# Performance work log

Measured on AMD Instinct MI355X. Metric: run time of the kernel, lower is better.

## Reference

```python
import jax, jax.numpy as jnp
import numpy as np

SIGMA_DATA = 16.0
ALPHA_BOND = 1.0


def safe_norm(x, axis=-1):
    # L2 norm with zero (sub)gradient at 0, matching torch.norm's behavior
    sq = jnp.sum(x * x, axis=axis)
    n = jnp.sqrt(jnp.where(sq > 0, sq, 1.0))
    return jnp.where(sq > 0, n, 0.0)


def weighted_rigid_align(x_l, xGT_l, w_l):
    # Aligns x_l onto xGT_l's frame (Kabsch with weights); output is detached.
    wm = w_l[..., None]                                   # [B,N,1]
    denom = jnp.sum(wm, axis=1, keepdims=True)
    mu = jnp.sum(wm * x_l, axis=1, keepdims=True) / denom
    muGT = jnp.sum(wm * xGT_l, axis=1, keepdims=True) / denom
    xc = x_l - mu
    xGTc = xGT_l - muGT
    # M = (w * xGT_c)^T @ x_c  -> [B,3,3]
    M = jnp.einsum('bni,bnj->bij', wm * xGTc, xc)
    U, S, Vh = jnp.linalg.svd(M)
    R = U @ Vh
    det = jnp.linalg.det(R)
    Fm = jnp.array([[1.0, 0.0, 0.0], [0.0, 1.0, 0.0], [0.0, 0.0, -1.0]], dtype=R.dtype)
    Rfix = jnp.einsum('bij,jk,bkl->bil', U, Fm, Vh)
    R = jnp.where(det[:, None, None] < 0, Rfix, R)
    xalign = xc @ jnp.swapaxes(R, -1, -2) + muGT
    return jax.lax.stop_gradient(xalign)


def diffusion_loss(xpred_l, xGT_l, ht, w_l):
    # Align ground truth onto prediction (note arg order in original forward)
    xGT_aligned = weighted_rigid_align(xGT_l, xpred_l, w_l)
    loss = jnp.sum(safe_norm(xpred_l - xGT_aligned) * w_l) / jnp.sum(w_l)
    if ALPHA_BOND > 0:
        w_pair = w_l[:, :, None] * w_l[:, None, :]                 # [B,N,N]
        d_pred = safe_norm(xpred_l[:, :, None] - xpred_l[:, None]) # [B,N,N]
        d_gt = safe_norm(xGT_l[:, :, None] - xGT_l[:, None])       # [B,N,N]
        L_bond = w_pair * (d_pred - d_gt) ** 2
        loss = loss + ALPHA_BOND * jnp.sum(L_bond) / jnp.sum(w_pair)
    return (ht ** 2 + SIGMA_DATA ** 2) / (ht + SIGMA_DATA) ** 2 * loss


def setup_inputs() -> dict:
    key = jax.random.key(0)
    k1, k2, k3, k4 = jax.random.split(key, 4)
    B, N = 4, 2048
    xpred_l = jax.random.normal(k1, (B, N, 3), dtype=jnp.float32) * 10.0
    xGT_l = jax.random.normal(k2, (B, N, 3), dtype=jnp.float32) * 10.0
    ht = jax.random.uniform(k3, (B,), dtype=jnp.float32, minval=0.1, maxval=4.0)
    w_l = jax.random.uniform(k4, (B, N), dtype=jnp.float32, minval=0.1, maxval=1.0)
    return {"xpred_l": xpred_l, "xGT_l": xGT_l, "ht": ht, "w_l": w_l}


def reference(xpred_l, xGT_l, ht, w_l):
    return diffusion_loss(xpred_l, xGT_l, ht, w_l)
```

## Files before the change

### kernel.cpp

```cpp
#include <hip/hip_runtime.h>
#include <math.h>


#define RT 256
#define CT 128
#define MAXB 8

__global__ __launch_bounds__(RT, 4)
void k_bond_stats(const float* __restrict__ pred, const float* __restrict__ gt,
                  const float* __restrict__ w, double* __restrict__ ws,
                  int N, int B, unsigned total) {
    const int b    = blockIdx.z;
    const int bx   = blockIdx.x;
    const int r0   = bx * RT;
    const int c0   = blockIdx.y * CT;
    const int tid  = threadIdx.x;
    const int lane = tid & 63, wave = tid >> 6;
    const int GX   = gridDim.x;
    const unsigned linear = (blockIdx.z * gridDim.y + blockIdx.y) * GX + blockIdx.x;

    double* statsSlot = ws;
    double* bondSlot  = ws + (size_t)B * GX * 16;

    if (blockIdx.x == 0 && blockIdx.y == 0 && blockIdx.z == 0 && tid == 0) {
        double* fin = bondSlot + total;
        fin[0] = 0.0; fin[1] = 0.0; fin[2] = 0.0;
    }

    const float* p  = pred + (size_t)b * N * 3;
    const float* g  = gt   + (size_t)b * N * 3;
    const float* wb = w    + (size_t)b * N;

    __shared__ float4 sp4[CT], sg4[CT];
    __shared__ double shred[4][16];

    const int  n      = r0 + tid;
    const bool row_ok = (n < N);
    float px=0.f,py=0.f,pz=0.f,gx=0.f,gy=0.f,gz=0.f,wn=0.f;
    if (row_ok) {
        px = p[3*n]; py = p[3*n+1]; pz = p[3*n+2];
        gx = g[3*n]; gy = g[3*n+1]; gz = g[3*n+2];
        wn = wb[n];
    }

    const bool bond_active = (c0 + CT > r0 + 1) && (c0 < N);
    float bond_f = 0.0f;
    if (bond_active) {
        for (int i = tid; i < CT; i += RT) {
            int m = c0 + i;
            float4 a = make_float4(0.f,0.f,0.f,0.f), c = a;
            if (m < N) {
                a = make_float4(p[3*m], p[3*m+1], p[3*m+2], wb[m]);
                c = make_float4(g[3*m], g[3*m+1], g[3*m+2], 0.f);
            }
            sp4[i] = a; sg4[i] = c;
        }
        __syncthreads();
        if (row_ok) {
            const int cc = min(CT, N - c0);
            if (c0 >= r0 + RT) {
                #pragma unroll 4
                for (int i = 0; i < cc; i++) {
                    float4 cp = sp4[i], cg = sg4[i];
                    float dxp=px-cp.x, dyp=py-cp.y, dzp=pz-cp.z;
                    float dxg=gx-cg.x, dyg=gy-cg.y, dzg=gz-cg.z;
                    float dp = sqrtf(dxp*dxp+dyp*dyp+dzp*dzp);
                    float dg = sqrtf(dxg*dxg+dyg*dyg+dzg*dzg);
                    float dd = dp - dg;
                    bond_f += (wn*cp.w)*(dd*dd);
                }
            } else if (n < c0 + cc - 1) {
                #pragma unroll 4
                for (int i = 0; i < cc; i++) {
                    float4 cp = sp4[i], cg = sg4[i];
                    float dxp=px-cp.x, dyp=py-cp.y, dzp=pz-cp.z;
                    float dxg=gx-cg.x, dyg=gy-cg.y, dzg=gz-cg.z;
                    float dp = sqrtf(dxp*dxp+dyp*dyp+dzp*dzp);
                    float dg = sqrtf(dxg*dxg+dyg*dyg+dzg*dzg);
                    float dd = dp - dg;
                    float t  = (wn*cp.w)*(dd*dd);
                    bond_f += (c0 + i > n) ? t : 0.0f;
                }
            }
        }
    }
    bond_f *= 2.0f;

    if (blockIdx.y == 0) {
        double wd=wn, pxd=px,pyd=py,pzd=pz, gxd=gx,gyd=gy,gzd=gz;
        double st[16] = {wd, wd*pxd, wd*pyd, wd*pzd, wd*gxd, wd*gyd, wd*gzd,
                         wd*pxd*gxd, wd*pxd*gyd, wd*pxd*gzd,
                         wd*pyd*gxd, wd*pyd*gyd, wd*pyd*gzd,
                         wd*pzd*gxd, wd*pzd*gyd, wd*pzd*gzd};
        #pragma unroll
        for (int off = 32; off > 0; off >>= 1) {
            #pragma unroll
            for (int k = 0; k < 16; k++) st[k] += __shfl_down(st[k], off, 64);
        }
        if (lane == 0) {
            #pragma unroll
            for (int k = 0; k < 16; k++) shred[wave][k] = st[k];
        }
        __syncthreads();
        if (tid < 16)
            statsSlot[((size_t)b*GX + bx)*16 + tid] =
                shred[0][tid]+shred[1][tid]+shred[2][tid]+shred[3][tid];
        __syncthreads();
    }

    double bd = (double)bond_f;
    #pragma unroll
    for (int off = 32; off > 0; off >>= 1) bd += __shfl_down(bd, off, 64);
    if (lane == 0) shred[wave][0] = bd;
    __syncthreads();
    if (tid == 0)
        bondSlot[linear] = shred[0][0]+shred[1][0]+shred[2][0]+shred[3][0];
}

__global__ __launch_bounds__(RT, 1)
void k_tail2(const float* __restrict__ pred, const float* __restrict__ gt,
             const float* __restrict__ ht, const float* __restrict__ w,
             float* __restrict__ out, double* __restrict__ ws,
             int N, int B, int GX, unsigned total, int AG) {
    const int tid  = threadIdx.x;
    const int lane = tid & 63, wave = tid >> 6;
    const double* statsSlot = ws;
    const double* bondSlot  = ws + (size_t)B * GX * 16;
    double* fin = (double*)(bondSlot + total);

    __shared__ double sstat[MAXB][16];
    __shared__ float  sR[MAXB][15];
    __shared__ double sW[MAXB];
    __shared__ double shredA[4], shredB[4];

    float htv[MAXB];
    if (tid == 0) {
        #pragma unroll
        for (int b2 = 0; b2 < MAXB; b2++) htv[b2] = (b2 < B) ? ht[b2] : 0.f;
    }

    if (tid < B * 16) {
        int bb = tid >> 4, k = tid & 15;
        double acc = 0.0;
        for (int j = 0; j < GX; j++) acc += statsSlot[((size_t)bb*GX + j)*16 + k];
        sstat[bb][k] = acc;
    }

    double bsum = 0.0;
    for (unsigned i = (unsigned)blockIdx.x * RT + tid; i < total; i += (unsigned)AG * RT)
        bsum += bondSlot[i];

    const int ptTotal = B * N;
    const int stride  = AG * RT;
    const int pt0     = blockIdx.x * RT + tid;
    const bool have0  = (pt0 < ptTotal);
    float px=0.f,py=0.f,pz=0.f,qx=0.f,qy=0.f,qz=0.f,wn=0.f;
    int b0 = 0;
    if (have0) {
        b0 = pt0 / N; int n0 = pt0 - b0 * N;
        const float* pp = pred + (size_t)b0 * N * 3;
        const float* gg = gt   + (size_t)b0 * N * 3;
        px = pp[3*n0]; py = pp[3*n0+1]; pz = pp[3*n0+2];
        qx = gg[3*n0]; qy = gg[3*n0+1]; qz = gg[3*n0+2];
        wn = w[(size_t)b0 * N + n0];
    }

    __syncthreads();

    if (tid < B) {
        const double* s = sstat[tid];
        double W = s[0];
        double mup[3] = { s[1]/W, s[2]/W, s[3]/W };
        double mug[3] = { s[4]/W, s[5]/W, s[6]/W };
        double M[3][3];
        for (int i = 0; i < 3; i++)
            for (int j = 0; j < 3; j++)
                M[i][j] = s[7 + i*3 + j] - W * mup[i] * mug[j];
        double A[3][3];
        for (int i = 0; i < 3; i++)
            for (int j = 0; j < 3; j++) {
                double t = 0.0;
                for (int k = 0; k < 3; k++) t += M[k][i] * M[k][j];
                A[i][j] = t;
            }
        double V[3][3] = {{1,0,0},{0,1,0},{0,0,1}};
        for (int sweep = 0; sweep < 6; sweep++) {
            for (int pq = 0; pq < 3; pq++) {
                int pp_ = (pq == 2) ? 1 : 0;
                int qq_ = (pq == 0) ? 1 : 2;
                double apq = A[pp_][qq_];
                if (fabs(apq) < 1e-300) continue;
                double app = A[pp_][pp_], aqq = A[qq_][qq_];
                double theta = (aqq - app) / (2.0 * apq);
                double t = copysign(1.0, theta) / (fabs(theta) + sqrt(theta*theta + 1.0));
                double cj = 1.0 / sqrt(t*t + 1.0), sn = t * cj;
                A[pp_][pp_] = app - t * apq;
                A[qq_][qq_] = aqq + t * apq;
                A[pp_][qq_] = A[qq_][pp_] = 0.0;
                int r = 3 - pp_ - qq_;
                double arp = A[r][pp_], arq = A[r][qq_];
                A[r][pp_] = A[pp_][r] = cj*arp - sn*arq;
                A[r][qq_] = A[qq_][r] = sn*arp + cj*arq;
                for (int rr = 0; rr < 3; rr++) {
                    double vp = V[rr][pp_], vq = V[rr][qq_];
                    V[rr][pp_] = cj*vp - sn*vq;
                    V[rr][qq_] = sn*vp + cj*vq;
                }
            }
        }
        double d[3] = { A[0][0], A[1][1], A[2][2] };
        int idx[3] = {0, 1, 2};
        for (int i = 0; i < 2; i++)
            for (int j = i + 1; j < 3; j++)
                if (d[idx[j]] > d[idx[i]]) { int tt = idx[i]; idx[i] = idx[j]; idx[j] = tt; }
        double u[3][3], v[3][3];
        for (int i = 0; i < 3; i++) {
            int c_ = idx[i];
            double sv = sqrt(fmax(d[c_], 0.0));
            double inv = (sv > 1e-12) ? 1.0 / sv : 0.0;
            for (int r = 0; r < 3; r++) v[i][r] = V[r][c_];
            for (int r = 0; r < 3; r++) {
                double t = 0.0;
                for (int k = 0; k < 3; k++) t += M[r][k] * v[i][k];
                u[i][r] = t * inv;
            }
        }
        double detM = M[0][0]*(M[1][1]*M[2][2] - M[1][2]*M[2][1])
                    - M[0][1]*(M[1][0]*M[2][2] - M[1][2]*M[2][0])
                    + M[0][2]*(M[1][0]*M[2][1] - M[1][1]*M[2][0]);
        double sg2 = (detM < 0.0) ? -1.0 : 1.0;
        for (int r = 0; r < 3; r++)
            for (int cc2 = 0; cc2 < 3; cc2++)
                sR[tid][r*3+cc2] = (float)(u[0][r]*v[0][cc2] + u[1][r]*v[1][cc2]
                                           + sg2 * u[2][r]*v[2][cc2]);
        for (int i = 0; i < 3; i++) sR[tid][9 + i]  = (float)mup[i];
        for (int i = 0; i < 3; i++) sR[tid][12 + i] = (float)mug[i];
        sW[tid] = W;
    }
    __syncthreads();

    double al = 0.0;
    if (have0) {
        const float* Rb = sR[b0];
        float x0 = qx - Rb[12], x1 = qy - Rb[13], x2 = qz - Rb[14];
        float ax = fmaf(Rb[0],x0, fmaf(Rb[1],x1, fmaf(Rb[2],x2, Rb[9])));
        float ay = fmaf(Rb[3],x0, fmaf(Rb[4],x1, fmaf(Rb[5],x2, Rb[10])));
        float az = fmaf(Rb[6],x0, fmaf(Rb[7],x1, fmaf(Rb[8],x2, Rb[11])));
        float ex = px-ax, ey = py-ay, ez = pz-az;
        al += (double)(wn * sqrtf(ex*ex + ey*ey + ez*ez));
    }
    for (int pt = pt0 + stride; pt < ptTotal; pt += stride) {
        int b2 = pt / N; int nn = pt - b2 * N;
        const float* pp = pred + (size_t)b2 * N * 3;
        const float* gg = gt   + (size_t)b2 * N * 3;
        const float* Rb = sR[b2];
        float x0 = gg[3*nn]-Rb[12], x1 = gg[3*nn+1]-Rb[13], x2 = gg[3*nn+2]-Rb[14];
        float ax = fmaf(Rb[0],x0, fmaf(Rb[1],x1, fmaf(Rb[2],x2, Rb[9])));
        float ay = fmaf(Rb[3],x0, fmaf(Rb[4],x1, fmaf(Rb[5],x2, Rb[10])));
        float az = fmaf(Rb[6],x0, fmaf(Rb[7],x1, fmaf(Rb[8],x2, Rb[11])));
        float ex = pp[3*nn]-ax, ey = pp[3*nn+1]-ay, ez = pp[3*nn+2]-az;
        al += (double)(w[(size_t)b2*N + nn] * sqrtf(ex*ex + ey*ey + ez*ez));
    }

    #pragma unroll
    for (int off = 32; off > 0; off >>= 1) {
        al   += __shfl_down(al,   off, 64);
        bsum += __shfl_down(bsum, off, 64);
    }
    if (lane == 0) { shredA[wave] = al; shredB[wave] = bsum; }
    __syncthreads();

    if (tid == 0) {
        double alB = shredA[0]+shredA[1]+shredA[2]+shredA[3];
        double bB  = shredB[0]+shredB[1]+shredB[2]+shredB[3];
        atomicAdd(&fin[0], alB);
        atomicAdd(&fin[1], bB);
        __threadfence();
        unsigned old = atomicAdd((unsigned int*)&fin[2], 1u);
        if (old == (unsigned)(AG - 1)) {
            double at = atomicAdd(&fin[0], 0.0);
            double bt = atomicAdd(&fin[1], 0.0);
            double tw = 0.0, twp = 0.0;
            for (int b2 = 0; b2 < B; b2++) { double W = sW[b2]; tw += W; twp += W*W; }
            double loss = at / tw + bt / twp;
            #pragma unroll
            for (int b2 = 0; b2 < MAXB; b2++) {
                if (b2 < B) {
                    double h = (double)htv[b2];
                    out[b2] = (float)(((h*h + 256.0) / ((h + 16.0)*(h + 16.0))) * loss);
                }
            }
        }
    }
}

extern "C" void kernel_launch(void* const* d_in, const int* in_sizes, int n_in,
                              void* d_out, int out_size, void* d_ws, size_t ws_size,
                              hipStream_t stream) {
    const float* pred = (const float*)d_in[0];
    const float* gt   = (const float*)d_in[1];
    const float* ht   = (const float*)d_in[2];
    const float* w    = (const float*)d_in[3];
    int B = in_sizes[2];
    int N = in_sizes[3] / B;
    double* ws = (double*)d_ws;
    float* out = (float*)d_out;

    int gx = (N + RT - 1) / RT;
    int gy = (N + CT - 1) / CT;
    unsigned total = (unsigned)(gx * gy * B);

    int ag = (B * N + RT - 1) / RT;
    if (ag > 64) ag = 64;
    if (ag < 1)  ag = 1;

    k_bond_stats<<<dim3(gx, gy, B), dim3(RT), 0, stream>>>(pred, gt, w, ws, N, B, total);
    k_tail2<<<dim3(ag), dim3(RT), 0, stream>>>(pred, gt, ht, w, out, ws, N, B, gx, total, ag);
}
```

Baseline: 97.52 us.

## Launch only upper-triangular square tiles and split columns across half-blocks

Replaces the rectangular 256x128 tile grid, where many lower-triangle blocks were launched only to exit, with a linear enumeration of upper-triangular 128x128 tiles. The tile index is decoded with a small loop, and the weighted-stats reduction moves to diagonal tiles. Each 256-thread block now covers 128 rows, with the two thread halves each taking 64 columns. The aim is to stop launching idle blocks, balance work across blocks and simplify the diagonal masking. In exchange, diagonal tiles still compute masked pairs, and the tail kernel now reads twice as many stats slots.

```diff
diff --git a/kernel.cpp b/kernel.cpp
--- a/kernel.cpp
+++ b/kernel.cpp
@@ -3,26 +3,26 @@
 
 
 #define RT 256
-#define CT 128
+#define TR 128
+#define TC 128
 #define MAXB 8
 
 __global__ __launch_bounds__(RT, 4)
 void k_bond_stats(const float* __restrict__ pred, const float* __restrict__ gt,
                   const float* __restrict__ w, double* __restrict__ ws,
-                  int N, int B, unsigned total) {
-    const int b    = blockIdx.z;
-    const int bx   = blockIdx.x;
-    const int r0   = bx * RT;
-    const int c0   = blockIdx.y * CT;
+                  int N, int B, int T, int CTILES, unsigned total) {
+    const int b    = blockIdx.y;
     const int tid  = threadIdx.x;
     const int lane = tid & 63, wave = tid >> 6;
-    const int GX   = gridDim.x;
-    const unsigned linear = (blockIdx.z * gridDim.y + blockIdx.y) * GX + blockIdx.x;
+
+    int rem = blockIdx.x, bx = 0;
+    while (rem >= CTILES - bx) { rem -= (CTILES - bx); bx++; }
+    const int by = bx + rem;
+    const int r0 = bx * TR, c0 = by * TC;
 
     double* statsSlot = ws;
-    double* bondSlot  = ws + (size_t)B * GX * 16;
-
-    if (blockIdx.x == 0 && blockIdx.y == 0 && blockIdx.z == 0 && tid == 0) {
+    double* bondSlot  = ws + (size_t)B * CTILES * 16;
+    if (blockIdx.x == 0 && blockIdx.y == 0 && tid == 0) {
         double* fin = bondSlot + total;
         fin[0] = 0.0; fin[1] = 0.0; fin[2] = 0.0;
     }
@@ -31,10 +31,12 @@
     const float* g  = gt   + (size_t)b * N * 3;
     const float* wb = w    + (size_t)b * N;
 
-    __shared__ float4 sp4[CT], sg4[CT];
+    __shared__ float4 sp4[TC], sg4[TC];
     __shared__ double shred[4][16];
 
-    const int  n      = r0 + tid;
+    const int rrow  = tid & (TR - 1);
+    const int rhalf = tid >> 7;
+    const int n     = r0 + rrow;
     const bool row_ok = (n < N);
     float px=0.f,py=0.f,pz=0.f,gx=0.f,gy=0.f,gz=0.f,wn=0.f;
     if (row_ok) {
@@ -43,51 +45,54 @@
         wn = wb[n];
     }
 
-    const bool bond_active = (c0 + CT > r0 + 1) && (c0 < N);
-    float bond_f = 0.0f;
-    if (bond_active) {
-        for (int i = tid; i < CT; i += RT) {
-            int m = c0 + i;
-            float4 a = make_float4(0.f,0.f,0.f,0.f), c = a;
-            if (m < N) {
-                a = make_float4(p[3*m], p[3*m+1], p[3*m+2], wb[m]);
-                c = make_float4(g[3*m], g[3*m+1], g[3*m+2], 0.f);
-            }
-            sp4[i] = a; sg4[i] = c;
-        }
-        __syncthreads();
-        if (row_ok) {
-            const int cc = min(CT, N - c0);
-            if (c0 >= r0 + RT) {
-                #pragma unroll 4
-                for (int i = 0; i < cc; i++) {
-                    float4 cp = sp4[i], cg = sg4[i];
-                    float dxp=px-cp.x, dyp=py-cp.y, dzp=pz-cp.z;
-                    float dxg=gx-cg.x, dyg=gy-cg.y, dzg=gz-cg.z;
-                    float dp = sqrtf(dxp*dxp+dyp*dyp+dzp*dzp);
-                    float dg = sqrtf(dxg*dxg+dyg*dyg+dzg*dzg);
-                    float dd = dp - dg;
-                    bond_f += (wn*cp.w)*(dd*dd);
-                }
-            } else if (n < c0 + cc - 1) {
-                #pragma unroll 4
-                for (int i = 0; i < cc; i++) {
-                    float4 cp = sp4[i], cg = sg4[i];
-                    float dxp=px-cp.x, dyp=py-cp.y, dzp=pz-cp.z;
-                    float dxg=gx-cg.x, dyg=gy-cg.y, dzg=gz-cg.z;
-                    float dp = sqrtf(dxp*dxp+dyp*dyp+dzp*dzp);
-                    float dg = sqrtf(dxg*dxg+dyg*dyg+dzg*dzg);
-                    float dd = dp - dg;
-                    float t  = (wn*cp.w)*(dd*dd);
-                    bond_f += (c0 + i > n) ? t : 0.0f;
-                }
-            }
-        }
-    }
-    bond_f *= 2.0f;
-
-    if (blockIdx.y == 0) {
-        double wd=wn, pxd=px,pyd=py,pzd=pz, gxd=gx,gyd=gy,gzd=gz;
+    {
+        int i = tid & (TC - 1);
+        int m = c0 + i;
+        if (tid < TC) {
+            float4 v = make_float4(0.f,0.f,0.f,0.f);
+            if (m < N) v = make_float4(p[3*m], p[3*m+1], p[3*m+2], wb[m]);
+            sp4[i] = v;
+        } else {
+            float4 v = make_float4(0.f,0.f,0.f,0.f);
+            if (m < N) v = make_float4(g[3*m], g[3*m+1], g[3*m+2], 0.f);
+            sg4[i] = v;
+        }
+    }
+    __syncthreads();
+
+    float acc = 0.f;
+    const int ib = rhalf * (TC / 2);
+    if (by > bx) {
+        #pragma unroll 4
+        for (int j = 0; j < TC/2; j++) {
+            int i = ib + j;
+            float4 cp = sp4[i], cg = sg4[i];
+            float dxp=px-cp.x, dyp=py-cp.y, dzp=pz-cp.z;
+            float dxg=gx-cg.x, dyg=gy-cg.y, dzg=gz-cg.z;
+            float dp = sqrtf(dxp*dxp+dyp*dyp+dzp*dzp);
+            float dg = sqrtf(dxg*dxg+dyg*dyg+dzg*dzg);
+            float dd = dp - dg;
+            acc = fmaf(cp.w, dd*dd, acc);
+        }
+    } else {
+        #pragma unroll 4
+        for (int j = 0; j < TC/2; j++) {
+            int i = ib + j;
+            float4 cp = sp4[i], cg = sg4[i];
+            float dxp=px-cp.x, dyp=py-cp.y, dzp=pz-cp.z;
+            float dxg=gx-cg.x, dyg=gy-cg.y, dzg=gz-cg.z;
+            float dp = sqrtf(dxp*dxp+dyp*dyp+dzp*dzp);
+            float dg = sqrtf(dxg*dxg+dyg*dyg+dzg*dzg);
+            float dd = dp - dg;
+            float t  = cp.w * (dd*dd);
+            acc += (i > rrow) ? t : 0.f;
+        }
+    }
+    float bond_f = 2.0f * wn * acc;
+
+    if (bx == by) {
+        double wd = (rhalf == 0) ? (double)wn : 0.0;
+        double pxd=px,pyd=py,pzd=pz, gxd=gx,gyd=gy,gzd=gz;
         double st[16] = {wd, wd*pxd, wd*pyd, wd*pzd, wd*gxd, wd*gyd, wd*gzd,
                          wd*pxd*gxd, wd*pxd*gyd, wd*pxd*gzd,
                          wd*pyd*gxd, wd*pyd*gyd, wd*pyd*gzd,
@@ -103,7 +108,7 @@
         }
         __syncthreads();
         if (tid < 16)
-            statsSlot[((size_t)b*GX + bx)*16 + tid] =
+            statsSlot[((size_t)b*CTILES + bx)*16 + tid] =
                 shred[0][tid]+shred[1][tid]+shred[2][tid]+shred[3][tid];
         __syncthreads();
     }
@@ -114,7 +119,8 @@
     if (lane == 0) shred[wave][0] = bd;
     __syncthreads();
     if (tid == 0)
-        bondSlot[linear] = shred[0][0]+shred[1][0]+shred[2][0]+shred[3][0];
+        bondSlot[(size_t)blockIdx.y * T + blockIdx.x] =
+            shred[0][0]+shred[1][0]+shred[2][0]+shred[3][0];
 }
 
 __global__ __launch_bounds__(RT, 1)
@@ -306,14 +312,14 @@
     double* ws = (double*)d_ws;
     float* out = (float*)d_out;
 
-    int gx = (N + RT - 1) / RT;
-    int gy = (N + CT - 1) / CT;
-    unsigned total = (unsigned)(gx * gy * B);
+    int CTILES = (N + TC - 1) / TC;
+    int T = CTILES * (CTILES + 1) / 2;
+    unsigned total = (unsigned)(B * T);
 
     int ag = (B * N + RT - 1) / RT;
     if (ag > 64) ag = 64;
     if (ag < 1)  ag = 1;
 
-    k_bond_stats<<<dim3(gx, gy, B), dim3(RT), 0, stream>>>(pred, gt, w, ws, N, B, total);
-    k_tail2<<<dim3(ag), dim3(RT), 0, stream>>>(pred, gt, ht, w, out, ws, N, B, gx, total, ag);
+    k_bond_stats<<<dim3(T, B), dim3(RT), 0, stream>>>(pred, gt, w, ws, N, B, T, CTILES, total);
+    k_tail2<<<dim3(ag), dim3(RT), 0, stream>>>(pred, gt, ht, w, out, ws, N, B, CTILES, total, ag);
 }
```

Result: faster. 95.28 us (-2.3%).
